# Kernel tuning notes

Hardware: AMD Instinct MI355X
Metric: run time of the kernel (lower is better)

Reference implementation:

```python
import jax, jax.numpy as jnp
import numpy as np

RADIUS = 6
KERNEL = 2 * RADIUS + 1  # 13
TEMPERATURE = 0.07
EPS = 1e-12  # F.normalize eps


def setup_inputs() -> dict:
    key = jax.random.key(0)
    k1, k2 = jax.random.split(key)
    B, C, H, W = 4, 256, 128, 128
    f_a = jax.random.normal(k1, (B, C, H, W), dtype=jnp.float32)
    f_b = jax.random.normal(k2, (B, C, H, W), dtype=jnp.float32)
    return {"f_a": f_a, "f_b": f_b}


def _l2_normalize(x):
    # matches F.normalize(x, dim=1): x / max(||x||_2, eps)
    n = jnp.sqrt(jnp.sum(x * x, axis=1, keepdims=True))
    return x / jnp.maximum(n, EPS)


def reference(f_a, f_b):
    a = _l2_normalize(f_a)
    b = _l2_normalize(f_b)
    b_pad = jnp.pad(b, ((0, 0), (0, 0), (RADIUS, RADIUS), (RADIUS, RADIUS)))

    # offsets in the same (row-major ky, kx) order as F.unfold
    ky, kx = jnp.meshgrid(jnp.arange(KERNEL), jnp.arange(KERNEL), indexing="ij")
    offsets = jnp.stack([ky.ravel(), kx.ravel()], axis=-1)  # [K^2, 2]

    shape = f_a.shape  # (B, C, H, W)

    def step(carry, off):
        shifted = jax.lax.dynamic_slice(b_pad, (0, 0, off[0], off[1]), shape)
        c = jnp.einsum("bchw,bchw->bhw", a, shifted)
        return carry, c

    _, corr = jax.lax.scan(step, None, offsets)  # [K^2, B, H, W]
    corr = jnp.transpose(corr, (1, 0, 2, 3)) / TEMPERATURE  # [B, K^2, H, W]
    return corr
```

## Files before the change

### kernel.cpp

```cpp
#include <hip/hip_runtime.h>


typedef _Float16 half8 __attribute__((ext_vector_type(8)));
typedef _Float16 half2v __attribute__((ext_vector_type(2)));
typedef float floatx4 __attribute__((ext_vector_type(4)));

#define B_ 4
#define C_ 256
#define H_ 128
#define W_ 128
#define K2_ 169
#define INV_T 14.285714285714286f

__global__ __launch_bounds__(256) void nt_kernel(const float* __restrict__ fa,
                                                 const float* __restrict__ fb,
                                                 _Float16* __restrict__ an,
                                                 _Float16* __restrict__ bn) {
  __shared__ _Float16 tile[256 * 66];
  __shared__ float ps[16 * 64];
  __shared__ float invn[64];
  const int bid = blockIdx.x;
  const int wh = bid & 1, h = (bid >> 1) & 127, bb = (bid >> 8) & 3, tens = bid >> 10;
  const float* __restrict__ src = tens ? fb : fa;
  _Float16* __restrict__ dst = tens ? bn : an;
  const int t = threadIdx.x;
  const int f = t & 15, cp = t >> 4;

  const float* gs = src + (((size_t)bb * C_ + cp) * H_ + h) * W_ + wh * 64 + f * 4;
  floatx4 ss = {0.f, 0.f, 0.f, 0.f};
  #pragma unroll
  for (int it = 0; it < 16; ++it) {
    const floatx4 v = *(const floatx4*)(gs + (size_t)it * 16 * H_ * W_);
    ss += v * v;
    const int c = it * 16 + cp;
    const int s8 = ((c >> 5) & 7) * 8;
    _Float16* wp = tile + c * 66 + ((f * 4) ^ s8);
    half2v p0 = {(_Float16)v.x, (_Float16)v.y};
    half2v p1 = {(_Float16)v.z, (_Float16)v.w};
    *(half2v*)wp = p0;
    *(half2v*)(wp + 2) = p1;
  }
  *(floatx4*)(ps + cp * 64 + f * 4) = ss;
  __syncthreads();
  if (t < 64) {
    float s2 = 0.f;
    #pragma unroll
    for (int p = 0; p < 16; ++p) s2 += ps[p * 64 + t];
    invn[t] = 1.0f / fmaxf(sqrtf(s2), 1e-12f);
  }
  __syncthreads();

  const int pr = t >> 3, seg = t & 7;
  const float inv0 = invn[2 * pr], inv1 = invn[2 * pr + 1];
  const int ppr = pr ^ (4 * seg);
  _Float16 o0[32] __attribute__((aligned(16)));
  _Float16 o1[32] __attribute__((aligned(16)));
  #pragma unroll
  for (int j = 0; j < 32; ++j) {
    const int c = seg * 32 + j;
    const half2v d = *(const half2v*)(tile + c * 66 + ppr * 2);
    o0[j] = (_Float16)((float)d.x * inv0);
    o1[j] = (_Float16)((float)d.y * inv1);
  }
  _Float16* dp = dst + (((size_t)bb * H_ + h) * W_ + wh * 64 + 2 * pr) * C_ + seg * 32;
  #pragma unroll
  for (int q4 = 0; q4 < 4; ++q4) {
    *(uint4*)(dp + q4 * 8) = *(const uint4*)(o0 + q4 * 8);
    *(uint4*)(dp + C_ + q4 * 8) = *(const uint4*)(o1 + q4 * 8);
  }
}

struct StageS { _Float16 a[2560]; _Float16 b[16384]; };
union SmemU { StageS s; float ostage[K2_ * 4 * 17]; };

__global__ __launch_bounds__(512, 4) void corr_kernel(const _Float16* __restrict__ an,
                                                      const _Float16* __restrict__ bn,
                                                      float* __restrict__ out) {
  __shared__ SmemU u;
  const int bid = blockIdx.x;
  const int xcd = bid & 7, l = bid >> 3;
  const int bb = l >> 5, hseg = (l >> 3) & 3, wt = l & 7;
  const int hg = xcd * 4 + hseg;
  const int h0 = hg * 4, w0 = wt * 16;
  const int t = threadIdx.x;
  const int lane = t & 63, wv = t >> 6;
  const int ml = lane & 15, q = lane >> 4;
  const int ntile = wv & 1, jjg = wv >> 1;

  _Float16* const smem = (_Float16*)&u.s;

  const _Float16* gptr[4];
  int loff[4];
  unsigned flags = 0u;
  #pragma unroll
  for (int j = 0; j < 4; ++j) {
    const int job = j * 512 + t;
    if (job < 1792) {
      const int sg = job / 448, px = job - sg * 448;
      const int row = px / 28, col = px - row * 28;
      const int rim = h0 - 6 + row, cim = w0 - 6 + col;
      const bool ok = ((unsigned)rim < (unsigned)H_) && ((unsigned)cim < (unsigned)W_);
      gptr[j] = bn + (((size_t)bb * H_ + (ok ? rim : 0)) * W_ + (ok ? cim : 0)) * C_ + sg * 8;
      loff[j] = 2560 + sg * 4096 + (row * 32 + col) * 8;
      if (ok) flags |= 1u << j;
    } else {
      const int jb = job - 1792;
      const int px = jb >> 2, sg = jb & 3;
      const int r = px >> 4, m = px & 15;
      gptr[j] = an + (((size_t)bb * H_ + h0 + r) * W_ + w0 + m) * C_ + sg * 8;
      loff[j] = px * 40 + sg * 8;
      flags |= 1u << j;
    }
  }

  floatx4 acc[4][4] = {};

  #pragma unroll
  for (int k0 = 0; k0 < C_; k0 += 32) {
    __syncthreads();
    #pragma unroll
    for (int j = 0; j < 4; ++j) {
      uint4 v = make_uint4(0u, 0u, 0u, 0u);
      if (flags & (1u << j)) v = *(const uint4*)(gptr[j] + k0);
      *(uint4*)(smem + loff[j]) = v;
    }
    __syncthreads();

    half8 A[4];
    #pragma unroll
    for (int r = 0; r < 4; ++r)
      A[r] = *(const half8*)(smem + (r * 16 + ml) * 40 + q * 8);

    #pragma unroll
    for (int uu = 0; uu < 4; ++uu) {
      const int jj = jjg + 4 * uu;
      const half8 Bf =
          *(const half8*)(smem + 2560 + q * 4096 + (jj * 32 + ntile * 16 + ml) * 8);
      #pragma unroll
      for (int r = 0; r < 4; ++r) {
        if ((uu == 0 && r > jjg) || (uu == 3 && r < jjg)) continue;
        acc[uu][r] = __builtin_amdgcn_mfma_f32_16x16x32_f16(A[r], Bf, acc[uu][r], 0, 0, 0);
      }
    }
  }
  __syncthreads();

  #pragma unroll
  for (int uu = 0; uu < 4; ++uu) {
    const int jj = jjg + 4 * uu;
    const int col = ntile * 16 + ml;
    #pragma unroll
    for (int r = 0; r < 4; ++r) {
      if ((uu == 0 && r > jjg) || (uu == 3 && r < jjg)) continue;
      const int dy6 = jj - r;
      #pragma unroll
      for (int p = 0; p < 4; ++p) {
        const int ip = q * 4 + p;
        const int dx6 = col - ip;
        if (dx6 >= 0 && dx6 <= 12)
          u.ostage[((dy6 * 13 + dx6) * 4 + r) * 17 + ip] = acc[uu][r][p] * INV_T;
      }
    }
  }
  __syncthreads();

  for (int sidx = t; sidx < K2_ * 64; sidx += 512) {
    const int k = sidx >> 6, rem = sidx & 63, r = rem >> 4, ip = rem & 15;
    out[(((size_t)bb * K2_ + k) * H_ + h0 + r) * W_ + w0 + ip] =
        u.ostage[(k * 4 + r) * 17 + ip];
  }
}

extern "C" void kernel_launch(void* const* d_in, const int* in_sizes, int n_in,
                              void* d_out, int out_size, void* d_ws, size_t ws_size,
                              hipStream_t stream) {
  const float* fa = (const float*)d_in[0];
  const float* fb = (const float*)d_in[1];
  float* out = (float*)d_out;
  _Float16* an = (_Float16*)d_ws;
  _Float16* bn = an + (size_t)B_ * H_ * W_ * C_;
  nt_kernel<<<2048, 256, 0, stream>>>(fa, fb, an, bn);
  corr_kernel<<<1024, 512, 0, stream>>>(an, bn, out);
}
```

Before: 247.7 us.

## Double-buffer corr tiles via direct global-to-LDS loads with channel-grouped layout

The normalized fp16 tensors are stored channel-grouped as [B][8][H][W][32], so each 32-channel K-step reads a contiguous block. The correlation kernel now loads tiles with global_load_lds straight into a double-buffered LDS stage, prefetching the next K-group while MFMAs run on the current one, and halves the output staging buffer by writing it in two passes. The 1/T scale is folded into the normalization of A. In exchange there is an extra zero-fill of LDS, more LDS use from double buffering, and slightly different fp16 rounding from the pre-scaled A values.

```diff
diff --git a/kernel.cpp b/kernel.cpp
--- a/kernel.cpp
+++ b/kernel.cpp
@@ -1,4 +1,5 @@
 #include <hip/hip_runtime.h>
+#include <stdint.h>
 
 
 typedef _Float16 half8 __attribute__((ext_vector_type(8)));
@@ -11,6 +12,12 @@
 #define W_ 128
 #define K2_ 169
 #define INV_T 14.285714285714286f
+#define KGS (H_ * W_ * 32)
+
+static __device__ __forceinline__ void gload16(const void* g, void* l) {
+  __builtin_amdgcn_global_load_lds((const __attribute__((address_space(1))) void*)g,
+                                   (__attribute__((address_space(3))) void*)l, 16, 0, 0);
+}
 
 __global__ __launch_bounds__(256) void nt_kernel(const float* __restrict__ fa,
                                                  const float* __restrict__ fb,
@@ -50,8 +57,9 @@
   }
   __syncthreads();
 
-  const int pr = t >> 3, seg = t & 7;
-  const float inv0 = invn[2 * pr], inv1 = invn[2 * pr + 1];
+  const int seg = t >> 5, pr = t & 31;
+  const float sc = tens ? 1.0f : INV_T;
+  const float inv0 = invn[2 * pr] * sc, inv1 = invn[2 * pr + 1] * sc;
   const int ppr = pr ^ (4 * seg);
   _Float16 o0[32] __attribute__((aligned(16)));
   _Float16 o1[32] __attribute__((aligned(16)));
@@ -62,16 +70,15 @@
     o0[j] = (_Float16)((float)d.x * inv0);
     o1[j] = (_Float16)((float)d.y * inv1);
   }
-  _Float16* dp = dst + (((size_t)bb * H_ + h) * W_ + wh * 64 + 2 * pr) * C_ + seg * 32;
+  _Float16* dp = dst + ((((size_t)bb * 8 + seg) * H_ + h) * W_ + wh * 64 + 2 * pr) * 32;
   #pragma unroll
   for (int q4 = 0; q4 < 4; ++q4) {
     *(uint4*)(dp + q4 * 8) = *(const uint4*)(o0 + q4 * 8);
-    *(uint4*)(dp + C_ + q4 * 8) = *(const uint4*)(o1 + q4 * 8);
-  }
-}
-
-struct StageS { _Float16 a[2560]; _Float16 b[16384]; };
-union SmemU { StageS s; float ostage[K2_ * 4 * 17]; };
+    *(uint4*)(dp + 32 + q4 * 8) = *(const uint4*)(o1 + q4 * 8);
+  }
+}
+
+union SmemU { _Float16 stage[2][16384]; float ostage[K2_ * 2 * 17]; };
 
 __global__ __launch_bounds__(512, 4) void corr_kernel(const _Float16* __restrict__ an,
                                                       const _Float16* __restrict__ bn,
@@ -87,55 +94,66 @@
   const int ml = lane & 15, q = lane >> 4;
   const int ntile = wv & 1, jjg = wv >> 1;
 
-  _Float16* const smem = (_Float16*)&u.s;
-
-  const _Float16* gptr[4];
-  int loff[4];
+  const _Float16* ptr[4];
   unsigned flags = 0u;
   #pragma unroll
   for (int j = 0; j < 4; ++j) {
     const int job = j * 512 + t;
     if (job < 1792) {
-      const int sg = job / 448, px = job - sg * 448;
-      const int row = px / 28, col = px - row * 28;
+      const int row = job / 112, rem = job - row * 112;
+      const int col = rem >> 2, qt = rem & 3;
       const int rim = h0 - 6 + row, cim = w0 - 6 + col;
       const bool ok = ((unsigned)rim < (unsigned)H_) && ((unsigned)cim < (unsigned)W_);
-      gptr[j] = bn + (((size_t)bb * H_ + (ok ? rim : 0)) * W_ + (ok ? cim : 0)) * C_ + sg * 8;
-      loff[j] = 2560 + sg * 4096 + (row * 32 + col) * 8;
+      ptr[j] = bn + (((size_t)bb * 8 * H_ + (ok ? rim : 0)) * W_ + (ok ? cim : 0)) * 32 + qt * 8;
       if (ok) flags |= 1u << j;
     } else {
-      const int jb = job - 1792;
-      const int px = jb >> 2, sg = jb & 3;
+      const int aj = job - 1792;
+      const int px = aj >> 2, qt = aj & 3;
       const int r = px >> 4, m = px & 15;
-      gptr[j] = an + (((size_t)bb * H_ + h0 + r) * W_ + w0 + m) * C_ + sg * 8;
-      loff[j] = px * 40 + sg * 8;
+      ptr[j] = an + (((size_t)bb * 8 * H_ + h0 + r) * W_ + w0 + m) * 32 + qt * 8;
       flags |= 1u << j;
     }
   }
 
+  const uint4 z4 = make_uint4(0u, 0u, 0u, 0u);
+  #pragma unroll
+  for (int j = 0; j < 4; ++j) {
+    *(uint4*)((char*)u.stage[0] + (j * 512 + t) * 16) = z4;
+    *(uint4*)((char*)u.stage[1] + (j * 512 + t) * 16) = z4;
+  }
+  __syncthreads();
+
+  #pragma unroll
+  for (int j = 0; j < 4; ++j) {
+    if (flags & (1u << j))
+      gload16(ptr[j], (char*)u.stage[0] + (j * 512 + wv * 64) * 16);
+    ptr[j] += KGS;
+  }
+
   floatx4 acc[4][4] = {};
 
-  #pragma unroll
-  for (int k0 = 0; k0 < C_; k0 += 32) {
+  for (int kg = 0; kg < 8; ++kg) {
     __syncthreads();
-    #pragma unroll
-    for (int j = 0; j < 4; ++j) {
-      uint4 v = make_uint4(0u, 0u, 0u, 0u);
-      if (flags & (1u << j)) v = *(const uint4*)(gptr[j] + k0);
-      *(uint4*)(smem + loff[j]) = v;
-    }
-    __syncthreads();
+    if (kg < 7) {
+      char* nb = (char*)u.stage[(kg + 1) & 1];
+      #pragma unroll
+      for (int j = 0; j < 4; ++j) {
+        if (flags & (1u << j))
+          gload16(ptr[j], nb + (j * 512 + wv * 64) * 16);
+        ptr[j] += KGS;
+      }
+    }
+    const _Float16* sb = u.stage[kg & 1];
 
     half8 A[4];
     #pragma unroll
     for (int r = 0; r < 4; ++r)
-      A[r] = *(const half8*)(smem + (r * 16 + ml) * 40 + q * 8);
+      A[r] = *(const half8*)(sb + 14336 + (r * 16 + ml) * 32 + q * 8);
 
     #pragma unroll
     for (int uu = 0; uu < 4; ++uu) {
       const int jj = jjg + 4 * uu;
-      const half8 Bf =
-          *(const half8*)(smem + 2560 + q * 4096 + (jj * 32 + ntile * 16 + ml) * 8);
+      const half8 Bf = *(const half8*)(sb + jj * 896 + (ntile * 16 + ml) * 32 + q * 8);
       #pragma unroll
       for (int r = 0; r < 4; ++r) {
         if ((uu == 0 && r > jjg) || (uu == 3 && r < jjg)) continue;
@@ -143,31 +161,33 @@
       }
     }
   }
-  __syncthreads();
-
-  #pragma unroll
-  for (int uu = 0; uu < 4; ++uu) {
-    const int jj = jjg + 4 * uu;
-    const int col = ntile * 16 + ml;
-    #pragma unroll
-    for (int r = 0; r < 4; ++r) {
-      if ((uu == 0 && r > jjg) || (uu == 3 && r < jjg)) continue;
-      const int dy6 = jj - r;
+
+  #pragma unroll
+  for (int r2 = 0; r2 < 2; ++r2) {
+    if (r2) __syncthreads();
+    #pragma unroll
+    for (int uu = 0; uu < 4; ++uu) {
+      const int jj = jjg + 4 * uu;
+      const int col = ntile * 16 + ml;
       #pragma unroll
-      for (int p = 0; p < 4; ++p) {
-        const int ip = q * 4 + p;
-        const int dx6 = col - ip;
-        if (dx6 >= 0 && dx6 <= 12)
-          u.ostage[((dy6 * 13 + dx6) * 4 + r) * 17 + ip] = acc[uu][r][p] * INV_T;
+      for (int rr = 2 * r2; rr < 2 * r2 + 2; ++rr) {
+        if ((uu == 0 && rr > jjg) || (uu == 3 && rr < jjg)) continue;
+        const int dy6 = jj - rr;
+        #pragma unroll
+        for (int p = 0; p < 4; ++p) {
+          const int ip = q * 4 + p;
+          const int dx6 = col - ip;
+          if (dx6 >= 0 && dx6 <= 12)
+            u.ostage[((dy6 * 13 + dx6) * 2 + (rr & 1)) * 17 + ip] = acc[uu][rr][p];
+        }
       }
     }
-  }
-  __syncthreads();
-
-  for (int sidx = t; sidx < K2_ * 64; sidx += 512) {
-    const int k = sidx >> 6, rem = sidx & 63, r = rem >> 4, ip = rem & 15;
-    out[(((size_t)bb * K2_ + k) * H_ + h0 + r) * W_ + w0 + ip] =
-        u.ostage[(k * 4 + r) * 17 + ip];
+    __syncthreads();
+    for (int s = t; s < K2_ * 32; s += 512) {
+      const int k = s >> 5, r1 = (s >> 4) & 1, ip = s & 15;
+      out[(((size_t)bb * K2_ + k) * H_ + h0 + 2 * r2 + r1) * W_ + w0 + ip] =
+          u.ostage[(k * 2 + r1) * 17 + ip];
+    }
   }
 }
 
```

After: 205.1 us. 17.2% less time.
